# Optimization experiments

Measured on AMD Instinct MI355X. Metric: run time of the kernel, lower is better.

## Reference

```python
import jax, jax.numpy as jnp
import numpy as np

ANCHORS = np.array([[116.0, 90.0], [156.0, 198.0], [373.0, 326.0]], dtype=np.float32)
NUM_CLASSES = 80
IMG_DIM = 608.0
NA = 3  # num anchors


def setup_inputs() -> dict:
    key = jax.random.key(0)
    # raw head output: [B, nA*(nC+6), G, G]
    x = jax.random.normal(key, (32, NA * (NUM_CLASSES + 6), 76, 76), dtype=jnp.float32)
    return {"x": x}


def reference(x):
    B, _, G, _ = x.shape
    stride = IMG_DIM / G
    # [B, A, G, G, nC+6]
    pred = x.reshape(B, NA, NUM_CLASSES + 6, G, G).transpose(0, 1, 3, 4, 2)
    px = jax.nn.sigmoid(pred[..., 0])
    py = jax.nn.sigmoid(pred[..., 1])
    pw = pred[..., 2]
    ph = pred[..., 3]
    pconf = jax.nn.sigmoid(pred[..., 4])
    pcls = jax.nn.sigmoid(pred[..., 5:])  # nC+1 channels (iou_aware=False path)

    grid_x = jnp.arange(G, dtype=x.dtype)[None, None, None, :]  # varies along last (i) axis
    grid_y = jnp.arange(G, dtype=x.dtype)[None, None, :, None]  # varies along row (j) axis
    scaled_anchors = jnp.asarray(ANCHORS, dtype=x.dtype) / stride
    anchor_w = scaled_anchors[:, 0].reshape(1, NA, 1, 1)
    anchor_h = scaled_anchors[:, 1].reshape(1, NA, 1, 1)

    pred_boxes = jnp.stack(
        [px + grid_x, py + grid_y, jnp.exp(pw) * anchor_w, jnp.exp(ph) * anchor_h],
        axis=-1,
    )  # [B, A, G, G, 4]

    n = NA * G * G
    out = jnp.concatenate(
        [
            pred_boxes.reshape(B, n, 4) * stride,
            pconf.reshape(B, n, 1),
            pcls.reshape(B, n, -1),
        ],
        axis=-1,
    )  # [B, nA*G*G, 4+1+(nC+1)]
    return out
```

## Files before the change

### kernel.cpp

```cpp
#include <hip/hip_runtime.h>
#include <cstdint>


#define GDIM 76
#define SP   (GDIM * GDIM)
#define NCH  86
#define NANC 3
#define TS   64
#define NV   (NCH * TS / 4)

typedef float v4f __attribute__((ext_vector_type(4)));

__global__ __launch_bounds__(256) void yolo_decode_kernel(
    const float* __restrict__ in, float* __restrict__ out) {
    __shared__ float tile[NCH][TS + 1];

    const int tid   = threadIdx.x;
    const int chunk = blockIdx.x;
    const int a     = blockIdx.y;
    const int b     = blockIdx.z;
    const int s0    = chunk * TS;
    const int valid = min(TS, SP - s0);

    const float* inp = in + ((size_t)(b * (NANC * NCH) + a * NCH)) * SP + s0;

    #pragma unroll
    for (int k = 0; k < 6; ++k) {
        const int idx = tid + (k << 8);
        if (idx < NV) {
            const int c  = idx >> 4;
            const int s4 = (idx & 15) << 2;
            if (s4 < valid) {
                const v4f v = *(const v4f*)(inp + (size_t)c * SP + s4);
                tile[c][s4 + 0] = v.x;
                tile[c][s4 + 1] = v.y;
                tile[c][s4 + 2] = v.z;
                tile[c][s4 + 3] = v.w;
            }
        }
    }
    __syncthreads();

    const float aw = (a == 0) ? 116.0f : (a == 1) ? 156.0f : 373.0f;
    const float ah = (a == 0) ?  90.0f : (a == 1) ? 198.0f : 326.0f;

    v4f* outp = (v4f*)(out + ((size_t)b * (NANC * SP) + (size_t)a * SP + (size_t)s0) * NCH);
    const int nvalid = (valid * NCH) >> 2;

    #pragma unroll
    for (int k = 0; k < 6; ++k) {
        const int v = tid + (k << 8);
        if (v < nvalid) {
            const int e0 = v << 2;
            const int s  = e0 / NCH;
            const int c0 = e0 - s * NCH;

            float vals[4];
            {
                int c = c0, ss = s;
                #pragma unroll
                for (int j = 0; j < 4; ++j) {
                    vals[j] = tile[c][ss];
                    ++c; if (c == NCH) { c = 0; ++ss; }
                }
            }

            v4f rr;
            {
                int c = c0, ss = s;
                #pragma unroll
                for (int j = 0; j < 4; ++j) {
                    const float x  = vals[j];
                    const float en = __expf(-x);
                    const float sg = __builtin_amdgcn_rcpf(1.0f + en);
                    float r = sg;
                    if (c < 4) {
                        const int sp_ = s0 + ss;
                        if      (c == 0) r = (sg + (float)(sp_ % GDIM)) * 8.0f;
                        else if (c == 1) r = (sg + (float)(sp_ / GDIM)) * 8.0f;
                        else if (c == 2) r = __builtin_amdgcn_rcpf(en) * aw;
                        else             r = __builtin_amdgcn_rcpf(en) * ah;
                    }
                    rr[j] = r;
                    ++c; if (c == NCH) { c = 0; ++ss; }
                }
            }
            __builtin_nontemporal_store(rr, outp + v);
        }
    }
}

extern "C" void kernel_launch(void* const* d_in, const int* in_sizes, int n_in,
                              void* d_out, int out_size, void* d_ws, size_t ws_size,
                              hipStream_t stream) {
    const float* in = (const float*)d_in[0];
    float* out = (float*)d_out;
    const int B = in_sizes[0] / (NANC * NCH * SP);
    dim3 grid((SP + TS - 1) / TS, NANC, B);
    yolo_decode_kernel<<<grid, 256, 0, stream>>>(in, out);
}
```

Measured before the change: 323.3 us.

## Issue all global loads up front, compute during staging, store via vector LDS reads

All six vector global loads are issued into registers before any LDS writes, so more memory traffic is in flight at once. The activation math now runs per channel in the load phase, where each thread's channel is uniform, which removes the per-element channel wrap and division logic from the store phase. The LDS tile is laid out spatial-major so the store phase reads aligned 16-byte vectors and writes them straight out. The trade-off is more registers held per thread and possible LDS bank conflicts from the strided scalar writes with stride NCH.

```diff
diff --git a/kernel.cpp b/kernel.cpp
--- a/kernel.cpp
+++ b/kernel.cpp
@@ -13,7 +13,7 @@
 
 __global__ __launch_bounds__(256) void yolo_decode_kernel(
     const float* __restrict__ in, float* __restrict__ out) {
-    __shared__ float tile[NCH][TS + 1];
+    __shared__ __align__(16) float tile[TS * NCH];
 
     const int tid   = threadIdx.x;
     const int chunk = blockIdx.x;
@@ -22,71 +22,67 @@
     const int s0    = chunk * TS;
     const int valid = min(TS, SP - s0);
 
+    const float aw = (a == 0) ? 116.0f : (a == 1) ? 156.0f : 373.0f;
+    const float ah = (a == 0) ?  90.0f : (a == 1) ? 198.0f : 326.0f;
+
     const float* inp = in + ((size_t)(b * (NANC * NCH) + a * NCH)) * SP + s0;
+
+    v4f vbuf[6];
+    #pragma unroll
+    for (int k = 0; k < 6; ++k) {
+        const int idx = tid + (k << 8);
+        const int c   = idx >> 4;
+        const int s4  = (idx & 15) << 2;
+        if (idx < NV && s4 < valid)
+            vbuf[k] = *(const v4f*)(inp + (size_t)c * SP + s4);
+    }
 
     #pragma unroll
     for (int k = 0; k < 6; ++k) {
         const int idx = tid + (k << 8);
-        if (idx < NV) {
-            const int c  = idx >> 4;
-            const int s4 = (idx & 15) << 2;
-            if (s4 < valid) {
-                const v4f v = *(const v4f*)(inp + (size_t)c * SP + s4);
-                tile[c][s4 + 0] = v.x;
-                tile[c][s4 + 1] = v.y;
-                tile[c][s4 + 2] = v.z;
-                tile[c][s4 + 3] = v.w;
+        const int c   = idx >> 4;
+        const int s4  = (idx & 15) << 2;
+        if (idx < NV && s4 < valid) {
+            v4f v = vbuf[k];
+            if (c >= 4) {
+                #pragma unroll
+                for (int j = 0; j < 4; ++j)
+                    v[j] = __builtin_amdgcn_rcpf(1.0f + __expf(-v[j]));
+            } else if (c == 0) {
+                const int sp_ = s0 + s4;
+                #pragma unroll
+                for (int j = 0; j < 4; ++j) {
+                    const float sg = __builtin_amdgcn_rcpf(1.0f + __expf(-v[j]));
+                    v[j] = (sg + (float)((sp_ + j) % GDIM)) * 8.0f;
+                }
+            } else if (c == 1) {
+                const int sp_ = s0 + s4;
+                #pragma unroll
+                for (int j = 0; j < 4; ++j) {
+                    const float sg = __builtin_amdgcn_rcpf(1.0f + __expf(-v[j]));
+                    v[j] = (sg + (float)((sp_ + j) / GDIM)) * 8.0f;
+                }
+            } else {
+                const float an = (c == 2) ? aw : ah;
+                #pragma unroll
+                for (int j = 0; j < 4; ++j)
+                    v[j] = __expf(v[j]) * an;
             }
+            #pragma unroll
+            for (int j = 0; j < 4; ++j)
+                tile[(s4 + j) * NCH + c] = v[j];
         }
     }
     __syncthreads();
 
-    const float aw = (a == 0) ? 116.0f : (a == 1) ? 156.0f : 373.0f;
-    const float ah = (a == 0) ?  90.0f : (a == 1) ? 198.0f : 326.0f;
-
     v4f* outp = (v4f*)(out + ((size_t)b * (NANC * SP) + (size_t)a * SP + (size_t)s0) * NCH);
     const int nvalid = (valid * NCH) >> 2;
-
+    const v4f* lv = (const v4f*)tile;
     #pragma unroll
     for (int k = 0; k < 6; ++k) {
         const int v = tid + (k << 8);
-        if (v < nvalid) {
-            const int e0 = v << 2;
-            const int s  = e0 / NCH;
-            const int c0 = e0 - s * NCH;
-
-            float vals[4];
-            {
-                int c = c0, ss = s;
-                #pragma unroll
-                for (int j = 0; j < 4; ++j) {
-                    vals[j] = tile[c][ss];
-                    ++c; if (c == NCH) { c = 0; ++ss; }
-                }
-            }
-
-            v4f rr;
-            {
-                int c = c0, ss = s;
-                #pragma unroll
-                for (int j = 0; j < 4; ++j) {
-                    const float x  = vals[j];
-                    const float en = __expf(-x);
-                    const float sg = __builtin_amdgcn_rcpf(1.0f + en);
-                    float r = sg;
-                    if (c < 4) {
-                        const int sp_ = s0 + ss;
-                        if      (c == 0) r = (sg + (float)(sp_ % GDIM)) * 8.0f;
-                        else if (c == 1) r = (sg + (float)(sp_ / GDIM)) * 8.0f;
-                        else if (c == 2) r = __builtin_amdgcn_rcpf(en) * aw;
-                        else             r = __builtin_amdgcn_rcpf(en) * ah;
-                    }
-                    rr[j] = r;
-                    ++c; if (c == NCH) { c = 0; ++ss; }
-                }
-            }
-            __builtin_nontemporal_store(rr, outp + v);
-        }
+        if (v < nvalid)
+            __builtin_nontemporal_store(lv[v], outp + v);
     }
 }
 
```

Measured after the change: 322.5 us. No clear change (-0.3%).
